# Optimization experiments

Measured on AMD Instinct MI355X. Metric: run time of the kernel, lower is better.

The kernel has to match this reference:

```python
import jax, jax.numpy as jnp
import numpy as np

B, L, D, H = 4, 1024, 768, 12
DH = D // H  # 64


def setup_inputs() -> dict:
    key = jax.random.key(0)
    kx, kk, kq, kv = jax.random.split(key, 4)
    # Original uses torch.rand (uniform [0,1)); scale by 1/D so pre-softmax
    # logits stay in a numerically sane range (same math, better conditioning).
    scale = 1.0 / D
    x = jax.random.normal(kx, (B, L, D), dtype=jnp.float32)
    k = jax.random.uniform(kk, (H, D, D), dtype=jnp.float32) * scale
    q = jax.random.uniform(kq, (H, D, D), dtype=jnp.float32) * scale
    v = jax.random.uniform(kv, (H, DH, D), dtype=jnp.float32) * scale
    return {"x": x, "k": k, "q": q, "v": v}


def reference(x, k, q, v):
    # x: [B, L, D]; torch permutes to [B, D, L] then 'bdl,ncd->bncl';
    # equivalent directly: 'bld,ncd->bncl'.
    K = jnp.einsum('bld,ncd->bncl', x, k)   # [B, H, D, L]
    Q = jnp.einsum('bld,ncd->bncl', x, q)   # [B, H, D, L]
    V = jnp.einsum('bld,ncd->bncl', x, v)   # [B, H, DH, L]
    scores = jnp.einsum('bndl,bndm->bnlm', Q, K)        # [B, H, L, L]
    S = jax.nn.softmax(scores, axis=-1)                  # softmax over dim 3
    R = jnp.einsum('bnkl,bndl->bndk', S, V)              # [B, H, DH, L]
    R = R.reshape(x.shape[0], D, -1)                     # [B, D, L]
    return jnp.transpose(R, (0, 2, 1))                   # [B, L, D]
```

## Files before the change

kernel.cpp:

```cpp
#include <hip/hip_runtime.h>
#include <hip/hip_bf16.h>
#include <stdint.h>
#include <stddef.h>

typedef unsigned short u16;
typedef __attribute__((ext_vector_type(8))) short short8;
typedef __attribute__((ext_vector_type(4))) float f32x4;
typedef __attribute__((ext_vector_type(16))) float f32x16;

#define NB 4
#define NL 1024
#define ND 768
#define NH 12
#define NDH 64

__device__ __forceinline__ u16 f2bf(float f) {
  __hip_bfloat16 h = __float2bfloat16(f);
  return *reinterpret_cast<u16*>(&h);
}
__device__ __forceinline__ float bf2f(u16 u) {
  __hip_bfloat16 h;
  *reinterpret_cast<u16*>(&h) = u;
  return __bfloat162float(h);
}

__device__ __forceinline__ void load16_to_lds(const u16* g, u16* l) {
  __builtin_amdgcn_global_load_lds(
      (__attribute__((address_space(1))) void*)(uintptr_t)g,
      (__attribute__((address_space(3))) void*)(uint32_t)(uintptr_t)l,
      16, 0, 0);
}

__global__ __launch_bounds__(256) void cast_bf16_kernel(const float* __restrict__ in,
                                                        u16* __restrict__ out, int n4) {
  int i = blockIdx.x * 256 + threadIdx.x;
  int stride = gridDim.x * 256;
  for (; i < n4; i += stride) {
    float4 f = ((const float4*)in)[i];
    ushort4 o;
    o.x = f2bf(f.x); o.y = f2bf(f.y); o.z = f2bf(f.z); o.w = f2bf(f.w);
    ((ushort4*)out)[i] = o;
  }
}

__global__ __launch_bounds__(256) void transpose_cast_kernel(const float* __restrict__ in,
                                                             u16* __restrict__ out) {
  __shared__ float tile[32][33];
  int h = blockIdx.z;
  const float* src = in + (size_t)h * ND * ND;
  u16* dst = out + (size_t)h * ND * ND;
  int c0 = blockIdx.x * 32, r0 = blockIdx.y * 32;
  int tx = threadIdx.x & 31, ty = threadIdx.x >> 5;
#pragma unroll
  for (int i = 0; i < 32; i += 8)
    tile[ty + i][tx] = src[(size_t)(r0 + ty + i) * ND + c0 + tx];
  __syncthreads();
#pragma unroll
  for (int i = 0; i < 32; i += 8)
    dst[(size_t)(c0 + ty + i) * ND + r0 + tx] = f2bf(tile[tx][ty + i]);
}

template <bool BF16_OUT, int IM, int IN, int KDIM, int LDC>
__global__ __launch_bounds__(256, 4) void gemm_bt(
    const u16* __restrict__ A, const u16* __restrict__ Bm, void* __restrict__ Cv,
    long sAb, long sAn, long sAz,
    long sBb, long sBn, long sBz,
    long sCb, long sCn, long sCz,
    int p0) {
  constexpr int BK = 64;
  constexpr int MTILE = IM * 64;
  constexpr int NTILE = IN * 64;
  constexpr int CPR = BK / 8;
  constexpr int ACH = MTILE * CPR / 256;
  constexpr int BCH = NTILE * CPR / 256;
  __shared__ __align__(16) u16 As[MTILE * BK];
  __shared__ __align__(16) u16 Bs[NTILE * BK];

  int id = blockIdx.x + gridDim.x * (blockIdx.y + gridDim.y * blockIdx.z);
  int total = gridDim.x * gridDim.y * gridDim.z;
  int xx, yy, zz;
  if ((total & 7) == 0) {
    int per = total >> 3;
    int wk = (id & 7) * per + (id >> 3);
    xx = wk % gridDim.x;
    int g2 = wk / gridDim.x;
    yy = g2 % gridDim.y;
    zz = g2 / gridDim.y;
  } else {
    xx = blockIdx.x; yy = blockIdx.y; zz = blockIdx.z;
  }

  int g = p0 + zz;
  int b = g / NH, n = g % NH;
  A  += (size_t)b * sAb + (size_t)n * sAn + (size_t)zz * sAz;
  Bm += (size_t)b * sBb + (size_t)n * sBn + (size_t)zz * sBz;
  size_t cOff = (size_t)b * sCb + (size_t)n * sCn + (size_t)zz * sCz;

  int m0 = yy * MTILE, n0 = xx * NTILE;
  int t = threadIdx.x;
  int lane = t & 63, w = t >> 6;
  int m32 = lane & 31, kg = lane >> 5;
  int wm = w >> 1, wn = w & 1;

  const u16* gAb;
  const u16* gBb;
  {
    int r = t / CPR;
    int cc = (t & (CPR - 1)) ^ (r & 7);
    gAb = A + (size_t)(m0 + r) * KDIM + cc * 8;
    gBb = Bm + (size_t)(n0 + r) * KDIM + cc * 8;
  }

  f32x16 acc[IM][IN];
#pragma unroll
  for (int i = 0; i < IM; i++)
#pragma unroll
    for (int j = 0; j < IN; j++)
#pragma unroll
      for (int r = 0; r < 16; r++) acc[i][j][r] = 0.f;

#pragma unroll 1
  for (int k0 = 0; k0 < KDIM; k0 += BK) {
    __syncthreads();
#pragma unroll
    for (int u = 0; u < ACH; u++)
      load16_to_lds(gAb + (size_t)u * 32 * KDIM, &As[(size_t)(u * 256 + w * 64) * 8]);
    gAb += BK;
#pragma unroll
    for (int u = 0; u < BCH; u++)
      load16_to_lds(gBb + (size_t)u * 32 * KDIM, &Bs[(size_t)(u * 256 + w * 64) * 8]);
    gBb += BK;
    __syncthreads();

#pragma unroll
    for (int kc = 0; kc < 2; kc++) {
      short8 af[IM][2], bfr[IN][2];
#pragma unroll
      for (int i = 0; i < IM; i++) {
        int row = wm * (IM * 32) + i * 32 + m32;
#pragma unroll
        for (int h = 0; h < 2; h++) {
          int ck = (kc * 4 + h * 2 + kg) ^ (row & 7);
          af[i][h] = *(const short8*)&As[row * BK + ck * 8];
        }
      }
#pragma unroll
      for (int j = 0; j < IN; j++) {
        int row = wn * (IN * 32) + j * 32 + m32;
#pragma unroll
        for (int h = 0; h < 2; h++) {
          int ck = (kc * 4 + h * 2 + kg) ^ (row & 7);
          bfr[j][h] = *(const short8*)&Bs[row * BK + ck * 8];
        }
      }
#pragma unroll
      for (int i = 0; i < IM; i++)
#pragma unroll
        for (int j = 0; j < IN; j++) {
          acc[i][j] = __builtin_amdgcn_mfma_f32_32x32x16_bf16(af[i][0], bfr[j][0], acc[i][j], 0, 0, 0);
          acc[i][j] = __builtin_amdgcn_mfma_f32_32x32x16_bf16(af[i][1], bfr[j][1], acc[i][j], 0, 0, 0);
        }
    }
  }

#pragma unroll
  for (int i = 0; i < IM; i++) {
#pragma unroll
    for (int j = 0; j < IN; j++) {
      int colg = n0 + wn * (IN * 32) + j * 32 + m32;
#pragma unroll
      for (int r = 0; r < 16; r++) {
        int rowg = m0 + wm * (IM * 32) + i * 32 + (r & 3) + 8 * (r >> 2) + 4 * kg;
        float vv = acc[i][j][r];
        if (BF16_OUT) {
          ((u16*)Cv)[cOff + (size_t)rowg * LDC + colg] = f2bf(vv);
        } else {
          ((float*)Cv)[cOff + (size_t)rowg * LDC + colg] = vv;
        }
      }
    }
  }
}

__global__ __launch_bounds__(256) void softmax_pv_kernel(
    const u16* __restrict__ Sb, const u16* __restrict__ V2, float* __restrict__ out,
    int p0) {
  __shared__ __align__(16) u16 Ps[64 * 128];
  __shared__ __align__(16) u16 Vs[64 * 128];

  int id = blockIdx.x + gridDim.x * blockIdx.y;
  int total = gridDim.x * gridDim.y;
  int xx, zz;
  if ((total & 7) == 0) {
    int per = total >> 3;
    int wk = (id & 7) * per + (id >> 3);
    xx = wk & 15; zz = wk >> 4;
  } else {
    xx = blockIdx.x; zz = blockIdx.y;
  }

  int g = p0 + zz;
  int b = g / NH, n = g % NH;
  const u16* S = Sb + (size_t)zz * NL * NL;
  const u16* V = V2 + (size_t)zz * NDH * NL;

  int l0 = xx * 64;
  int t = threadIdx.x;
  int lane = t & 63, w = t >> 6;
  int row16 = lane & 15, q = lane >> 4;
  int rs = row16 & 7;

  f32x4 acc[5];
#pragma unroll
  for (int j = 0; j < 5; j++) acc[j] = (f32x4){0.f, 0.f, 0.f, 0.f};

  short8 onesf;
  {
    short val = (row16 == 0) ? (short)0x3F80 : (short)0;
#pragma unroll
    for (int e = 0; e < 8; e++) onesf[e] = val;
  }

  const u16* ssrc[4];
  const u16* vsrc[4];
#pragma unroll
  for (int u = 0; u < 4; u++) {
    int c = u * 256 + t;
    int r = c >> 4, cc = (c & 15) ^ (r & 7);
    ssrc[u] = S + (size_t)(l0 + r) * NL + cc * 8;
    vsrc[u] = V + (size_t)r * NL + cc * 8;
  }

#pragma unroll 1
  for (int mt = 0; mt < 8; mt++) {
    int mo = mt * 128;
    __syncthreads();
#pragma unroll
    for (int u = 0; u < 4; u++)
      load16_to_lds(ssrc[u] + mo, &Ps[(size_t)(u * 256 + w * 64) * 8]);
#pragma unroll
    for (int u = 0; u < 4; u++)
      load16_to_lds(vsrc[u] + mo, &Vs[(size_t)(u * 256 + w * 64) * 8]);
    __syncthreads();

#pragma unroll
    for (int kk = 0; kk < 4; kk++) {
      int ch = ((kk * 4 + q) ^ rs) * 16;
      int lrow = w * 16 + row16;
      short8 raw = *(const short8*)((const char*)Ps + lrow * 256 + ch);
      short8 af;
#pragma unroll
      for (int e = 0; e < 8; e++) af[e] = (short)f2bf(__expf(bf2f((u16)raw[e])));
      short8 bfr[4];
#pragma unroll
      for (int j = 0; j < 4; j++) {
        int dh = j * 16 + row16;
        bfr[j] = *(const short8*)((const char*)Vs + dh * 256 + ch);
      }
#pragma unroll
      for (int j = 0; j < 4; j++)
        acc[j] = __builtin_amdgcn_mfma_f32_16x16x32_bf16(af, bfr[j], acc[j], 0, 0, 0);
      acc[4] = __builtin_amdgcn_mfma_f32_16x16x32_bf16(af, onesf, acc[4], 0, 0, 0);
    }
  }

#pragma unroll
  for (int r = 0; r < 4; r++) {
    float sum = __shfl(acc[4][r], lane & 48, 64);
    float inv = 1.0f / sum;
    int row = l0 + w * 16 + q * 4 + r;
    float* op = out + ((size_t)b * NL + row) * ND + n * NDH;
#pragma unroll
    for (int j = 0; j < 4; j++)
      op[j * 16 + row16] = acc[j][r] * inv;
  }
}

extern "C" void kernel_launch(void* const* d_in, const int* in_sizes, int n_in,
                              void* d_out, int out_size, void* d_ws, size_t ws_size,
                              hipStream_t stream) {
  (void)in_sizes; (void)n_in; (void)out_size;
  const float* x  = (const float*)d_in[0];
  const float* kI = (const float*)d_in[1];
  const float* qI = (const float*)d_in[2];
  const float* vI = (const float*)d_in[3];
  float* out = (float*)d_out;

  size_t off = 0;
  char* wsb = (char*)d_ws;
  auto alloc = [&](size_t bytes) -> char* {
    char* p = wsb + off;
    off += (bytes + 255) & ~(size_t)255;
    return p;
  };
  u16* xb = (u16*)alloc((size_t)NB * NL * ND * 2);
  u16* qT = (u16*)alloc((size_t)NH * ND * ND * 2);
  u16* kT = (u16*)alloc((size_t)NH * ND * ND * 2);
  u16* vb = (u16*)alloc((size_t)NH * NDH * ND * 2);
  u16* MT = (u16*)alloc((size_t)NH * ND * ND * 2);
  size_t fixedSz = off;
  const size_t perPair = (size_t)NL * ND * 2 + (size_t)NL * NL * 2 + (size_t)NDH * NL * 2;
  int chunk = NB * NH;
  if (fixedSz + (size_t)chunk * perPair > ws_size) {
    size_t avail = ws_size > fixedSz ? ws_size - fixedSz : 0;
    chunk = (int)(avail / perPair);
    if (chunk < 1) chunk = 1;
    if (chunk > NB * NH) chunk = NB * NH;
  }
  u16* T  = (u16*)alloc((size_t)chunk * NL * ND * 2);
  u16* Sb = (u16*)alloc((size_t)chunk * NL * NL * 2);
  u16* V2 = (u16*)alloc((size_t)chunk * NDH * NL * 2);

  const long DD  = (long)ND * ND;
  const long LD  = (long)NL * ND;
  const long LL  = (long)NL * NL;
  const long DHD = (long)NDH * ND;
  const long DHL = (long)NDH * NL;

  {
    int n4 = NB * NL * ND / 4;
    cast_bf16_kernel<<<dim3((n4 + 255) / 256), dim3(256), 0, stream>>>(x, xb, n4);
    int n4v = NH * NDH * ND / 4;
    cast_bf16_kernel<<<dim3((n4v + 255) / 256), dim3(256), 0, stream>>>(vI, vb, n4v);
  }
  transpose_cast_kernel<<<dim3(24, 24, NH), dim3(256), 0, stream>>>(qI, qT);
  transpose_cast_kernel<<<dim3(24, 24, NH), dim3(256), 0, stream>>>(kI, kT);

  gemm_bt<true, 2, 2, 768, ND><<<dim3(6, 6, NH), dim3(256), 0, stream>>>(
      kT, qT, MT,
      0, DD, 0,  0, DD, 0,  0, DD, 0, 0);

  for (int p0 = 0; p0 < NB * NH; p0 += chunk) {
    int c = NB * NH - p0;
    if (c > chunk) c = chunk;
    gemm_bt<true, 1, 1, 768, NL><<<dim3(16, 1, c), dim3(256), 0, stream>>>(
        vb, xb, V2,
        0, DHD, 0,  LD, 0, 0,  0, 0, DHL, p0);
    gemm_bt<true, 2, 2, 768, ND><<<dim3(6, 8, c), dim3(256), 0, stream>>>(
        xb, MT, T,
        LD, 0, 0,  0, DD, 0,  0, 0, LD, p0);
    gemm_bt<true, 2, 2, 768, NL><<<dim3(8, 8, c), dim3(256), 0, stream>>>(
        T, xb, Sb,
        0, 0, LD,  LD, 0, 0,  0, 0, LL, p0);
    softmax_pv_kernel<<<dim3(16, c), dim3(256), 0, stream>>>(Sb, V2, out, p0);
  }
}
```

Measured before the change: 316.1 us.

## Add 256x256 pipelined MFMA GEMM and batch V projection and transposes

Adds a new 512-thread GEMM kernel with 256x256 output tiles, double-buffered LDS filled by direct global-to-LDS loads, XOR-swizzled LDS layout and priority-raised MFMA phases. It replaces the two large per-pair GEMMs (x·M and T·x^T), aiming for more operand reuse and higher MFMA utilisation. The V projection moves out of the chunk loop into one GEMM over all heads per batch, and the two q/k transpose-cast launches merge into one, cutting launch count and small-grid inefficiency. In exchange, the V2 buffer is now held for all pairs, and the large tiles give fewer blocks (48 or 64 per pair), so occupancy or wave quantisation could suffer.

```diff
diff --git a/kernel.cpp b/kernel.cpp
--- a/kernel.cpp
+++ b/kernel.cpp
@@ -43,12 +43,15 @@
   }
 }
 
-__global__ __launch_bounds__(256) void transpose_cast_kernel(const float* __restrict__ in,
-                                                             u16* __restrict__ out) {
+__global__ __launch_bounds__(256) void transpose_cast2_kernel(const float* __restrict__ qI,
+                                                              const float* __restrict__ kI,
+                                                              u16* __restrict__ qT,
+                                                              u16* __restrict__ kTp) {
   __shared__ float tile[32][33];
-  int h = blockIdx.z;
-  const float* src = in + (size_t)h * ND * ND;
-  u16* dst = out + (size_t)h * ND * ND;
+  int hz = blockIdx.z;
+  int h = (hz < NH) ? hz : hz - NH;
+  const float* src = ((hz < NH) ? qI : kI) + (size_t)h * ND * ND;
+  u16* dst = ((hz < NH) ? qT : kTp) + (size_t)h * ND * ND;
   int c0 = blockIdx.x * 32, r0 = blockIdx.y * 32;
   int tx = threadIdx.x & 31, ty = threadIdx.x >> 5;
 #pragma unroll
@@ -182,6 +185,170 @@
   }
 }
 
+template <bool BF16_OUT, int KDIM, int LDC>
+__global__ __launch_bounds__(512, 2) void gemm256_bt(
+    const u16* __restrict__ A, const u16* __restrict__ Bm, void* __restrict__ Cv,
+    long sAb, long sAn, long sAz,
+    long sBb, long sBn, long sBz,
+    long sCb, long sCn, long sCz,
+    int p0) {
+  constexpr int BK = 64;
+  constexpr int NT = KDIM / BK;
+  static_assert(KDIM % BK == 0 && NT >= 3, "pipeline needs >=3 K-tiles");
+  __shared__ __align__(16) u16 As[2][256 * BK];
+  __shared__ __align__(16) u16 Bs[2][256 * BK];
+
+  int id = blockIdx.x + gridDim.x * (blockIdx.y + gridDim.y * blockIdx.z);
+  int total = gridDim.x * gridDim.y * gridDim.z;
+  int xx, yy, zz;
+  if ((total & 7) == 0) {
+    int per = total >> 3;
+    int wk = (id & 7) * per + (id >> 3);
+    xx = wk % gridDim.x;
+    int g2 = wk / gridDim.x;
+    yy = g2 % gridDim.y;
+    zz = g2 / gridDim.y;
+  } else {
+    xx = blockIdx.x; yy = blockIdx.y; zz = blockIdx.z;
+  }
+
+  int g = p0 + zz;
+  int b = g / NH, n = g % NH;
+  A  += (size_t)b * sAb + (size_t)n * sAn + (size_t)zz * sAz;
+  Bm += (size_t)b * sBb + (size_t)n * sBn + (size_t)zz * sBz;
+  size_t cOff = (size_t)b * sCb + (size_t)n * sCn + (size_t)zz * sCz;
+
+  int m0 = yy * 256, n0 = xx * 256;
+  int t = threadIdx.x;
+  int lane = t & 63, w = t >> 6;
+  int wm = w >> 2, wn = w & 3;
+  int l15 = lane & 15, q4 = lane >> 4;
+
+  int r0 = t >> 3;
+  int cc0 = (t & 7) ^ (r0 & 7);
+  const u16* gA = A + (size_t)(m0 + r0) * KDIM + cc0 * 8;
+  const u16* gB = Bm + (size_t)(n0 + r0) * KDIM + cc0 * 8;
+
+  u16* Ac = &As[0][0]; u16* Ao = &As[1][0];
+  u16* Bc = &Bs[0][0]; u16* Bo = &Bs[1][0];
+  int ldsOff = w * 64 * 8;
+
+#define STG_A(dst, k0, u) load16_to_lds(gA + (size_t)(u) * 64 * KDIM + (k0), (dst) + (u) * 512 * 8 + ldsOff)
+#define STG_B(dst, k0, u) load16_to_lds(gB + (size_t)(u) * 64 * KDIM + (k0), (dst) + (u) * 512 * 8 + ldsOff)
+
+#define READ_A(buf, H, dst) do { \
+  _Pragma("unroll") for (int fm = 0; fm < 4; fm++) { \
+    int row = (H) * 128 + wm * 64 + fm * 16 + l15; \
+    _Pragma("unroll") for (int ks = 0; ks < 2; ks++) { \
+      int ck = (ks * 4 + q4) ^ (row & 7); \
+      dst[fm][ks] = *(const short8*)((buf) + row * 64 + ck * 8); \
+    } \
+  } \
+} while (0)
+
+#define READ_B(buf, G, dst) do { \
+  _Pragma("unroll") for (int fn = 0; fn < 2; fn++) { \
+    int row = (G) * 128 + wn * 32 + fn * 16 + l15; \
+    _Pragma("unroll") for (int ks = 0; ks < 2; ks++) { \
+      int ck = (ks * 4 + q4) ^ (row & 7); \
+      dst[fn][ks] = *(const short8*)((buf) + row * 64 + ck * 8); \
+    } \
+  } \
+} while (0)
+
+#define MFMA_PH(H, G, AR, BR) do { \
+  __builtin_amdgcn_s_setprio(1); \
+  _Pragma("unroll") for (int ks = 0; ks < 2; ks++) \
+    _Pragma("unroll") for (int fm = 0; fm < 4; fm++) \
+      _Pragma("unroll") for (int fn = 0; fn < 2; fn++) \
+        acc[H][G][fm][fn] = __builtin_amdgcn_mfma_f32_16x16x32_bf16(AR[fm][ks], BR[fn][ks], acc[H][G][fm][fn], 0, 0, 0); \
+  __builtin_amdgcn_s_setprio(0); \
+} while (0)
+
+  f32x4 acc[2][2][4][2];
+#pragma unroll
+  for (int h = 0; h < 2; h++)
+#pragma unroll
+    for (int gg = 0; gg < 2; gg++)
+#pragma unroll
+      for (int fm = 0; fm < 4; fm++)
+#pragma unroll
+        for (int fn = 0; fn < 2; fn++)
+          acc[h][gg][fm][fn] = (f32x4){0.f, 0.f, 0.f, 0.f};
+
+  STG_A(Ac, 0, 0); STG_A(Ac, 0, 1); STG_A(Ac, 0, 2); STG_A(Ac, 0, 3);
+  STG_B(Bc, 0, 0); STG_B(Bc, 0, 1); STG_B(Bc, 0, 2); STG_B(Bc, 0, 3);
+  STG_A(Ao, BK, 0); STG_A(Ao, BK, 1);
+  asm volatile("s_waitcnt vmcnt(2)" ::: "memory");
+  __builtin_amdgcn_s_barrier();
+  __builtin_amdgcn_sched_barrier(0);
+
+#pragma unroll 1
+  for (int tk = 0; tk < NT; ++tk) {
+    short8 af[4][2], bf0[2][2], bf1[2][2];
+    if (tk + 1 < NT) {
+      int kn1 = (tk + 1) * BK;
+      STG_A(Ao, kn1, 2); STG_A(Ao, kn1, 3);
+      STG_B(Bo, kn1, 0); STG_B(Bo, kn1, 1); STG_B(Bo, kn1, 2); STG_B(Bo, kn1, 3);
+    }
+    READ_A(Ac, 0, af);
+    READ_B(Bc, 0, bf0);
+    MFMA_PH(0, 0, af, bf0);
+    READ_B(Bc, 1, bf1);
+    MFMA_PH(0, 1, af, bf1);
+    __builtin_amdgcn_sched_barrier(0);
+    asm volatile("s_waitcnt lgkmcnt(0)" ::: "memory");
+    __builtin_amdgcn_s_barrier();
+    __builtin_amdgcn_sched_barrier(0);
+    if (tk + 2 < NT) {
+      int kn2 = (tk + 2) * BK;
+      STG_A(Ac, kn2, 0); STG_A(Ac, kn2, 1);
+    }
+    READ_A(Ac, 1, af);
+    MFMA_PH(1, 0, af, bf0);
+    MFMA_PH(1, 1, af, bf1);
+    if (tk + 1 < NT) {
+      __builtin_amdgcn_sched_barrier(0);
+      asm volatile("s_waitcnt lgkmcnt(0)" ::: "memory");
+      if (tk + 2 < NT) {
+        asm volatile("s_waitcnt vmcnt(2)" ::: "memory");
+      } else {
+        asm volatile("s_waitcnt vmcnt(0)" ::: "memory");
+      }
+      __builtin_amdgcn_s_barrier();
+      __builtin_amdgcn_sched_barrier(0);
+    }
+    u16* tp = Ac; Ac = Ao; Ao = tp;
+    tp = Bc; Bc = Bo; Bo = tp;
+  }
+
+#pragma unroll
+  for (int h = 0; h < 2; h++)
+#pragma unroll
+    for (int gg = 0; gg < 2; gg++)
+#pragma unroll
+      for (int fm = 0; fm < 4; fm++)
+#pragma unroll
+        for (int fn = 0; fn < 2; fn++) {
+          int colg = n0 + gg * 128 + wn * 32 + fn * 16 + l15;
+#pragma unroll
+          for (int r = 0; r < 4; r++) {
+            int rowg = m0 + h * 128 + wm * 64 + fm * 16 + q4 * 4 + r;
+            float vv = acc[h][gg][fm][fn][r];
+            if (BF16_OUT) {
+              ((u16*)Cv)[cOff + (size_t)rowg * LDC + colg] = f2bf(vv);
+            } else {
+              ((float*)Cv)[cOff + (size_t)rowg * LDC + colg] = vv;
+            }
+          }
+        }
+#undef STG_A
+#undef STG_B
+#undef READ_A
+#undef READ_B
+#undef MFMA_PH
+}
+
 __global__ __launch_bounds__(256) void softmax_pv_kernel(
     const u16* __restrict__ Sb, const u16* __restrict__ V2, float* __restrict__ out,
     int p0) {
@@ -202,7 +369,7 @@
   int g = p0 + zz;
   int b = g / NH, n = g % NH;
   const u16* S = Sb + (size_t)zz * NL * NL;
-  const u16* V = V2 + (size_t)zz * NDH * NL;
+  const u16* V = V2 + (size_t)g * NDH * NL;
 
   int l0 = xx * 64;
   int t = threadIdx.x;
@@ -298,8 +465,9 @@
   u16* kT = (u16*)alloc((size_t)NH * ND * ND * 2);
   u16* vb = (u16*)alloc((size_t)NH * NDH * ND * 2);
   u16* MT = (u16*)alloc((size_t)NH * ND * ND * 2);
+  u16* V2 = (u16*)alloc((size_t)NB * NH * NDH * NL * 2);
   size_t fixedSz = off;
-  const size_t perPair = (size_t)NL * ND * 2 + (size_t)NL * NL * 2 + (size_t)NDH * NL * 2;
+  const size_t perPair = (size_t)NL * ND * 2 + (size_t)NL * NL * 2;
   int chunk = NB * NH;
   if (fixedSz + (size_t)chunk * perPair > ws_size) {
     size_t avail = ws_size > fixedSz ? ws_size - fixedSz : 0;
@@ -309,12 +477,10 @@
   }
   u16* T  = (u16*)alloc((size_t)chunk * NL * ND * 2);
   u16* Sb = (u16*)alloc((size_t)chunk * NL * NL * 2);
-  u16* V2 = (u16*)alloc((size_t)chunk * NDH * NL * 2);
 
   const long DD  = (long)ND * ND;
   const long LD  = (long)NL * ND;
   const long LL  = (long)NL * NL;
-  const long DHD = (long)NDH * ND;
   const long DHL = (long)NDH * NL;
 
   {
@@ -323,23 +489,23 @@
     int n4v = NH * NDH * ND / 4;
     cast_bf16_kernel<<<dim3((n4v + 255) / 256), dim3(256), 0, stream>>>(vI, vb, n4v);
   }
-  transpose_cast_kernel<<<dim3(24, 24, NH), dim3(256), 0, stream>>>(qI, qT);
-  transpose_cast_kernel<<<dim3(24, 24, NH), dim3(256), 0, stream>>>(kI, kT);
+  transpose_cast2_kernel<<<dim3(24, 24, 2 * NH), dim3(256), 0, stream>>>(qI, kI, qT, kT);
 
   gemm_bt<true, 2, 2, 768, ND><<<dim3(6, 6, NH), dim3(256), 0, stream>>>(
       kT, qT, MT,
       0, DD, 0,  0, DD, 0,  0, DD, 0, 0);
 
+  gemm_bt<true, 2, 2, 768, NL><<<dim3(8, 6, NB), dim3(256), 0, stream>>>(
+      vb, xb, V2,
+      0, 0, 0,  0, 0, LD,  0, 0, (long)NH * DHL, 0);
+
   for (int p0 = 0; p0 < NB * NH; p0 += chunk) {
     int c = NB * NH - p0;
     if (c > chunk) c = chunk;
-    gemm_bt<true, 1, 1, 768, NL><<<dim3(16, 1, c), dim3(256), 0, stream>>>(
-        vb, xb, V2,
-        0, DHD, 0,  LD, 0, 0,  0, 0, DHL, p0);
-    gemm_bt<true, 2, 2, 768, ND><<<dim3(6, 8, c), dim3(256), 0, stream>>>(
+    gemm256_bt<true, 768, ND><<<dim3(3, 4, c), dim3(512), 0, stream>>>(
         xb, MT, T,
         LD, 0, 0,  0, DD, 0,  0, 0, LD, p0);
-    gemm_bt<true, 2, 2, 768, NL><<<dim3(8, 8, c), dim3(256), 0, stream>>>(
+    gemm256_bt<true, 768, NL><<<dim3(4, 4, c), dim3(512), 0, stream>>>(
         T, xb, Sb,
         0, 0, LD,  LD, 0, 0,  0, 0, LL, p0);
     softmax_pv_kernel<<<dim3(16, c), dim3(256), 0, stream>>>(Sb, V2, out, p0);
```

Measured after the change: 315.7 us. No clear change (-0.1%).
